# Kernel optimization log

Measured on AMD Instinct MI355X. Metric: run time of the kernel, lower is better.

Reference implementation:

```python
import jax, jax.numpy as jnp
import numpy as np

ROPE_BASE = 10000.0
NEG_INF = -1e30


def _rope(x, positions):
    """x: [B, heads, D]; positions: [B] int. Matches PrecomputedRotaryEmbedding
    with emb = cat(freqs, freqs) and rotate-half."""
    D = x.shape[-1]
    half = D // 2
    inv_freq = 1.0 / (ROPE_BASE ** (jnp.arange(0, D, 2, dtype=jnp.float32) / D))  # [D/2]
    freqs = positions.astype(jnp.float32)[:, None] * inv_freq[None, :]            # [B, D/2]
    emb = jnp.concatenate([freqs, freqs], axis=-1)                                # [B, D]
    cos = jnp.cos(emb)[:, None, :]
    sin = jnp.sin(emb)[:, None, :]
    x1, x2 = x[..., :half], x[..., half:]
    rotated = jnp.concatenate([-x2, x1], axis=-1)
    return x * cos + rotated * sin


def setup_inputs() -> dict:
    key = jax.random.key(0)
    ks = jax.random.split(key, 6)
    B, H, Hkv, D = 32, 32, 8, 128
    block_size, max_blocks = 16, 256
    num_blocks = B * max_blocks  # 8192, disjoint blocks per sequence
    return {
        "query": jax.random.normal(ks[0], (B, H, D), dtype=jnp.float32),
        "key": jax.random.normal(ks[1], (B, Hkv, D), dtype=jnp.float32),
        "value": jax.random.normal(ks[2], (B, Hkv, D), dtype=jnp.float32),
        "k_cache": jax.random.normal(ks[3], (num_blocks, block_size, Hkv, D), dtype=jnp.float32),
        "v_cache": jax.random.normal(ks[4], (num_blocks, block_size, Hkv, D), dtype=jnp.float32),
        "block_table": jnp.arange(B * max_blocks, dtype=jnp.int32).reshape(B, max_blocks),
        "context_lens": jax.random.randint(ks[5], (B,), 1, 4096, dtype=jnp.int32),
        "block_size": block_size,
    }


def reference(query, key, value, k_cache, v_cache, block_table, context_lens, block_size):
    B, H, D = query.shape
    Hkv = key.shape[1]
    G = H // Hkv
    num_blocks, bs = k_cache.shape[0], k_cache.shape[1]
    scale = D ** -0.5

    # 1) RoPE at position = context_len (as in the original forward)
    q = _rope(query, context_lens)                      # [B, H, D]
    k_new = _rope(key, context_lens)                    # [B, Hkv, D]

    # 2) scatter-store new KV at slot of token (context_len - 1)
    last = context_lens - 1
    slots = block_table[jnp.arange(B), last // block_size] * block_size + last % block_size
    kc = k_cache.reshape(num_blocks * bs, Hkv, D).at[slots].set(k_new)
    vc = v_cache.reshape(num_blocks * bs, Hkv, D).at[slots].set(value)
    kc = kc.reshape(num_blocks, bs, Hkv, D)
    vc = vc.reshape(num_blocks, bs, Hkv, D)

    # 3) gather paged KV per sequence via block_table
    S = block_table.shape[1] * bs                       # max seq len
    Kg = kc[block_table].reshape(B, S, Hkv, D)          # [B, S, Hkv, D]
    Vg = vc[block_table].reshape(B, S, Hkv, D)

    # 4) GQA attention over valid positions [0, context_len)
    qg = q.reshape(B, Hkv, G, D)
    scores = jnp.einsum('bkgd,bskd->bkgs', qg, Kg) * scale   # [B, Hkv, G, S]
    valid = (jnp.arange(S)[None, :] < context_lens[:, None])  # [B, S]
    scores = jnp.where(valid[:, None, None, :], scores, NEG_INF)
    probs = jax.nn.softmax(scores, axis=-1)
    out = jnp.einsum('bkgs,bskd->bkgd', probs, Vg).reshape(B, H, D)
    return out
```

## Files before the change

### kernel.cpp

```cpp
#include <hip/hip_runtime.h>
#include <math.h>

namespace {
constexpr int B   = 32;
constexpr int H   = 32;
constexpr int HKV = 8;
constexpr int D   = 128;
constexpr int G   = H / HKV;
constexpr int BS  = 16;
constexpr int MAXB = 256;
constexpr int S   = BS * MAXB;
constexpr float SCALE = 0.08838834764831845f;
}

__global__ void rope_kernel(const float* __restrict__ query,
                            const float* __restrict__ key,
                            const int*   __restrict__ ctx,
                            float* __restrict__ q_out,
                            float* __restrict__ k_out)
{
    const int row = blockIdx.x;
    const int t   = threadIdx.x;
    const bool is_q = row < B * H;
    const float* src;
    float* dst;
    int b;
    if (is_q) { b = row / H;  src = query + (size_t)row * D; dst = q_out + (size_t)row * D; }
    else      { int r = row - B * H; b = r / HKV;
                src = key + (size_t)r * D;  dst = k_out + (size_t)r * D; }
    const float pos = (float)ctx[b];
    const float inv = powf(10000.0f, -(2.0f * t) / (float)D);
    const float f = pos * inv;
    const float c = cosf(f), s = sinf(f);
    const float x1 = src[t], x2 = src[t + 64];
    float o1 = x1 * c - x2 * s;
    float o2 = x2 * c + x1 * s;
    if (is_q) { o1 *= SCALE; o2 *= SCALE; }
    dst[t]      = o1;
    dst[t + 64] = o2;
}

__global__ __launch_bounds__(256, 8)
void attn_kernel(const float* __restrict__ qr,
                 const float* __restrict__ kr,
                 const float* __restrict__ vnew,
                 const float* __restrict__ kc,
                 const float* __restrict__ vc,
                 const int*   __restrict__ bt,
                 const int*   __restrict__ ctx,
                 float* __restrict__ pl,
                 float* __restrict__ pa,
                 int chunk, int nch)
{
    const int c  = blockIdx.x;
    const int kv = blockIdx.y;
    const int b  = blockIdx.z;
    const int len = ctx[b];
    const int start = c * chunk;
    if (start >= len) return;
    const int end = min(start + chunk, len);
    const int lim = (end == len) ? len - 1 : end;

    const int tid  = threadIdx.x;
    const int wave = tid >> 6;
    const int half = (tid >> 5) & 1;
    const int sgp  = tid >> 5;
    const int t    = tid & 31;

    float4 q[G];
    {
        const float* qbase = qr + ((size_t)b * H + kv * G) * D + t * 4;
        #pragma unroll
        for (int g = 0; g < G; ++g)
            q[g] = *reinterpret_cast<const float4*>(qbase + g * D);
    }

    float l[G];
    float4 acc[G];
    #pragma unroll
    for (int g = 0; g < G; ++g) {
        l[g] = 0.f;
        acc[g] = make_float4(0.f, 0.f, 0.f, 0.f);
    }

    const int* btb = bt + b * MAXB + (start >> 4);
    const int e[4] = { btb[0], btb[1], btb[2], btb[3] };

    auto rowbase = [&](int k) -> size_t {
        const int slot = sgp + 8 * (k & 1);
        return ((size_t)(e[k >> 1] * BS + slot) * HKV + kv) * D + t * 4;
    };

    auto process = [&](const float4& k4, const float4& v4) {
        #pragma unroll
        for (int g = 0; g < G; ++g) {
            float s = q[g].x * k4.x + q[g].y * k4.y + q[g].z * k4.z + q[g].w * k4.w;
            s += __shfl_xor(s, 1);
            s += __shfl_xor(s, 2);
            s += __shfl_xor(s, 4);
            s += __shfl_xor(s, 8);
            s += __shfl_xor(s, 16);
            const float pv = __expf(s);
            l[g] += pv;
            acc[g].x += pv * v4.x;
            acc[g].y += pv * v4.y;
            acc[g].z += pv * v4.z;
            acc[g].w += pv * v4.w;
        }
    };

    const int pw = start + sgp;
    float4 kk, vv;
    {
        const size_t r0 = rowbase(0);
        if (pw < lim) {
            kk = *reinterpret_cast<const float4*>(kc + r0);
            vv = *reinterpret_cast<const float4*>(vc + r0);
        }
    }
    #pragma unroll
    for (int k = 1; k < 8; ++k) {
        if (pw + 8 * k < lim) {
            const size_t rk = rowbase(k);
            const float4 kn = *reinterpret_cast<const float4*>(kc + rk);
            const float4 vn = *reinterpret_cast<const float4*>(vc + rk);
            process(kk, vv);
            kk = kn; vv = vn;
        }
    }
    if (pw < lim) process(kk, vv);

    if (end == len && ((len - 1 - start) & 7) == sgp) {
        const size_t off = ((size_t)b * HKV + kv) * D + t * 4;
        const float4 k4 = *reinterpret_cast<const float4*>(kr + off);
        const float4 v4 = *reinterpret_cast<const float4*>(vnew + off);
        process(k4, v4);
    }

    #pragma unroll
    for (int g = 0; g < G; ++g) {
        l[g] += __shfl_xor(l[g], 32);
        acc[g].x += __shfl_xor(acc[g].x, 32);
        acc[g].y += __shfl_xor(acc[g].y, 32);
        acc[g].z += __shfl_xor(acc[g].z, 32);
        acc[g].w += __shfl_xor(acc[g].w, 32);
    }

    __shared__ float sm_l[4][G];
    __shared__ float sm_acc[4][G][D];
    if (half == 0) {
        #pragma unroll
        for (int g = 0; g < G; ++g) {
            if (t == 0) sm_l[wave][g] = l[g];
            *reinterpret_cast<float4*>(&sm_acc[wave][g][t * 4]) = acc[g];
        }
    }
    __syncthreads();

    for (int idx = tid; idx < G * D; idx += 256) {
        const int g = idx >> 7, d = idx & 127;
        const float A = sm_acc[0][g][d] + sm_acc[1][g][d] +
                        sm_acc[2][g][d] + sm_acc[3][g][d];
        const size_t pi = (((size_t)b * HKV + kv) * nch + c) * G + g;
        if (d == 0)
            pl[pi] = sm_l[0][g] + sm_l[1][g] + sm_l[2][g] + sm_l[3][g];
        pa[pi * D + d] = A;
    }
}

__global__ void combine_kernel(const float* __restrict__ pl,
                               const float* __restrict__ pa,
                               const int*   __restrict__ ctx,
                               float* __restrict__ out,
                               int chunk, int nch)
{
    const int bk = blockIdx.x;
    const int b  = bk / HKV;
    const int kv = bk % HKV;
    const int len = ctx[b];
    const int nc = min(nch, (len + chunk - 1) / chunk);
    const int g = threadIdx.x >> 7;
    const int d = threadIdx.x & 127;

    const size_t base = (((size_t)b * HKV + kv) * nch) * G + g;
    float L = 0.f, A = 0.f;
    for (int c = 0; c < nc; ++c) {
        const size_t pi = base + (size_t)c * G;
        L += pl[pi];
        A += pa[pi * D + d];
    }
    out[((size_t)b * H + kv * G + g) * D + d] = A / L;
}

extern "C" void kernel_launch(void* const* d_in, const int* in_sizes, int n_in,
                              void* d_out, int out_size, void* d_ws, size_t ws_size,
                              hipStream_t stream) {
    const float* query   = (const float*)d_in[0];
    const float* key     = (const float*)d_in[1];
    const float* value   = (const float*)d_in[2];
    const float* k_cache = (const float*)d_in[3];
    const float* v_cache = (const float*)d_in[4];
    const int*   bt      = (const int*)d_in[5];
    const int*   ctx     = (const int*)d_in[6];
    float* out = (float*)d_out;
    float* ws  = (float*)d_ws;

    float* qr = ws;
    float* kr = qr + (size_t)B * H * D;
    float* pbase = kr + (size_t)B * HKV * D;
    const size_t fixed_bytes = ((size_t)B * H * D + (size_t)B * HKV * D) * 4;

    int chunk = 64;
    int nch = (S + chunk - 1) / chunk;
    auto need = [&](int n) {
        return fixed_bytes + (size_t)B * HKV * n * G * (1 + D) * 4;
    };
    while (need(nch) > ws_size && chunk < S) {
        chunk *= 2;
        nch = (S + chunk - 1) / chunk;
    }

    float* pl = pbase;
    float* pa = pl + (size_t)B * HKV * nch * G;

    rope_kernel<<<B * (H + HKV), 64, 0, stream>>>(query, key, ctx, qr, kr);

    dim3 grid(nch, HKV, B);
    attn_kernel<<<grid, 256, 0, stream>>>(qr, kr, value, k_cache, v_cache,
                                          bt, ctx, pl, pa, chunk, nch);

    combine_kernel<<<B * HKV, 512, 0, stream>>>(pl, pa, ctx, out, chunk, nch);
}
```

Before: 151.5 us.

## Restructure attention into single-wave blocks covering two KV heads per chunk

Each attention block becomes a single 64-lane wave, where each half-wave handles one KV head and walks all tokens of the chunk sequentially. This drops the shared-memory cross-wave reduction and __syncthreads. The default chunk shrinks to 32 so more blocks are launched, and the workspace fallback now stops growing the chunk at 64. In exchange each block runs a serial token loop with lower memory-level parallelism, and the combine kernel has more partials to reduce. If the workspace is small, the capped chunk size could overflow it.

```diff
diff --git a/kernel.cpp b/kernel.cpp
--- a/kernel.cpp
+++ b/kernel.cpp
@@ -40,7 +40,7 @@
     dst[t + 64] = o2;
 }
 
-__global__ __launch_bounds__(256, 8)
+__global__ __launch_bounds__(64, 4)
 void attn_kernel(const float* __restrict__ qr,
                  const float* __restrict__ kr,
                  const float* __restrict__ vnew,
@@ -52,20 +52,19 @@
                  float* __restrict__ pa,
                  int chunk, int nch)
 {
-    const int c  = blockIdx.x;
-    const int kv = blockIdx.y;
-    const int b  = blockIdx.z;
+    const int c = blockIdx.x;
+    const int y = blockIdx.y;
+    const int b = blockIdx.z;
     const int len = ctx[b];
     const int start = c * chunk;
     if (start >= len) return;
     const int end = min(start + chunk, len);
     const int lim = (end == len) ? len - 1 : end;
 
-    const int tid  = threadIdx.x;
-    const int wave = tid >> 6;
-    const int half = (tid >> 5) & 1;
-    const int sgp  = tid >> 5;
-    const int t    = tid & 31;
+    const int lane = threadIdx.x;
+    const int half = lane >> 5;
+    const int t    = lane & 31;
+    const int kv   = 2 * y + half;
 
     float4 q[G];
     {
@@ -83,12 +82,16 @@
         acc[g] = make_float4(0.f, 0.f, 0.f, 0.f);
     }
 
-    const int* btb = bt + b * MAXB + (start >> 4);
-    const int e[4] = { btb[0], btb[1], btb[2], btb[3] };
-
-    auto rowbase = [&](int k) -> size_t {
-        const int slot = sgp + 8 * (k & 1);
-        return ((size_t)(e[k >> 1] * BS + slot) * HKV + kv) * D + t * 4;
+    const int* btb  = bt + b * MAXB + (start >> 4);
+    const int  maxe = 255 - (start >> 4);
+    int e[4];
+    #pragma unroll
+    for (int j = 0; j < 4; ++j) e[j] = btb[min(j, maxe)];
+
+    const int laneoff = y * 2 * D + half * D + t * 4;
+
+    auto rowaddr = [&](int i) -> size_t {
+        return ((size_t)(e[i >> 4] * BS + (i & 15))) * (HKV * D) + laneoff;
     };
 
     auto process = [&](const float4& k4, const float4& v4) {
@@ -109,28 +112,23 @@
         }
     };
 
-    const int pw = start + sgp;
+    const int n = lim - start;
     float4 kk, vv;
-    {
-        const size_t r0 = rowbase(0);
-        if (pw < lim) {
-            kk = *reinterpret_cast<const float4*>(kc + r0);
-            vv = *reinterpret_cast<const float4*>(vc + r0);
-        }
-    }
-    #pragma unroll
-    for (int k = 1; k < 8; ++k) {
-        if (pw + 8 * k < lim) {
-            const size_t rk = rowbase(k);
-            const float4 kn = *reinterpret_cast<const float4*>(kc + rk);
-            const float4 vn = *reinterpret_cast<const float4*>(vc + rk);
-            process(kk, vv);
-            kk = kn; vv = vn;
-        }
-    }
-    if (pw < lim) process(kk, vv);
-
-    if (end == len && ((len - 1 - start) & 7) == sgp) {
+    if (n > 0) {
+        const size_t a0 = rowaddr(0);
+        kk = *reinterpret_cast<const float4*>(kc + a0);
+        vv = *reinterpret_cast<const float4*>(vc + a0);
+    }
+    for (int i = 1; i < n; ++i) {
+        const size_t ai = rowaddr(i);
+        const float4 kn = *reinterpret_cast<const float4*>(kc + ai);
+        const float4 vn = *reinterpret_cast<const float4*>(vc + ai);
+        process(kk, vv);
+        kk = kn; vv = vn;
+    }
+    if (n > 0) process(kk, vv);
+
+    if (end == len) {
         const size_t off = ((size_t)b * HKV + kv) * D + t * 4;
         const float4 k4 = *reinterpret_cast<const float4*>(kr + off);
         const float4 v4 = *reinterpret_cast<const float4*>(vnew + off);
@@ -139,32 +137,9 @@
 
     #pragma unroll
     for (int g = 0; g < G; ++g) {
-        l[g] += __shfl_xor(l[g], 32);
-        acc[g].x += __shfl_xor(acc[g].x, 32);
-        acc[g].y += __shfl_xor(acc[g].y, 32);
-        acc[g].z += __shfl_xor(acc[g].z, 32);
-        acc[g].w += __shfl_xor(acc[g].w, 32);
-    }
-
-    __shared__ float sm_l[4][G];
-    __shared__ float sm_acc[4][G][D];
-    if (half == 0) {
-        #pragma unroll
-        for (int g = 0; g < G; ++g) {
-            if (t == 0) sm_l[wave][g] = l[g];
-            *reinterpret_cast<float4*>(&sm_acc[wave][g][t * 4]) = acc[g];
-        }
-    }
-    __syncthreads();
-
-    for (int idx = tid; idx < G * D; idx += 256) {
-        const int g = idx >> 7, d = idx & 127;
-        const float A = sm_acc[0][g][d] + sm_acc[1][g][d] +
-                        sm_acc[2][g][d] + sm_acc[3][g][d];
         const size_t pi = (((size_t)b * HKV + kv) * nch + c) * G + g;
-        if (d == 0)
-            pl[pi] = sm_l[0][g] + sm_l[1][g] + sm_l[2][g] + sm_l[3][g];
-        pa[pi * D + d] = A;
+        if (t == 0) pl[pi] = l[g];
+        *reinterpret_cast<float4*>(pa + pi * D + t * 4) = acc[g];
     }
 }
 
@@ -210,12 +185,12 @@
     float* pbase = kr + (size_t)B * HKV * D;
     const size_t fixed_bytes = ((size_t)B * H * D + (size_t)B * HKV * D) * 4;
 
-    int chunk = 64;
+    int chunk = 32;
     int nch = (S + chunk - 1) / chunk;
     auto need = [&](int n) {
         return fixed_bytes + (size_t)B * HKV * n * G * (1 + D) * 4;
     };
-    while (need(nch) > ws_size && chunk < S) {
+    while (need(nch) > ws_size && chunk < 64) {
         chunk *= 2;
         nch = (S + chunk - 1) / chunk;
     }
@@ -225,9 +200,9 @@
 
     rope_kernel<<<B * (H + HKV), 64, 0, stream>>>(query, key, ctx, qr, kr);
 
-    dim3 grid(nch, HKV, B);
-    attn_kernel<<<grid, 256, 0, stream>>>(qr, kr, value, k_cache, v_cache,
-                                          bt, ctx, pl, pa, chunk, nch);
+    dim3 grid(nch, 4, B);
+    attn_kernel<<<grid, 64, 0, stream>>>(qr, kr, value, k_cache, v_cache,
+                                         bt, ctx, pl, pa, chunk, nch);
 
     combine_kernel<<<B * HKV, 512, 0, stream>>>(pl, pa, ctx, out, chunk, nch);
 }
```

Result: slower. 169.9 us (+12.2%).
